# Performance work log

Hardware: AMD Instinct MI355X
Metric: run time of the kernel (lower is better)

Reference implementation:

```python
import jax, jax.numpy as jnp
import numpy as np

P = 4096      # particles per event
F = 128       # max features per particle (inner ragged axis)
H = 128       # hidden_size


def setup_inputs() -> dict:
    key = jax.random.key(0)
    ks = jax.random.split(key, 12)
    s = 1.0 / np.sqrt(H)  # torch RNN default init scale
    u = lambda k, shp: jax.random.uniform(k, shp, jnp.float32, -s, s)
    event = jax.random.normal(ks[0], (P, F, 1), jnp.float32)
    lengths = jnp.maximum(1, jax.random.randint(ks[1], (P,), 0, F))  # ragged lengths in [1, F)
    return {
        "event": event,
        "lengths": lengths,
        "W_ih1": u(ks[2], (H, 1)), "W_hh1": u(ks[3], (H, H)),
        "b_ih1": u(ks[4], (H,)),   "b_hh1": u(ks[5], (H,)),
        "W_ih2": u(ks[6], (H, H)), "W_hh2": u(ks[7], (H, H)),
        "b_ih2": u(ks[8], (H,)),   "b_hh2": u(ks[9], (H,)),
    }


def reference(event, lengths, W_ih1, W_hh1, b_ih1, b_hh1,
              W_ih2, W_hh2, b_ih2, b_hh2):
    # net1: vanilla tanh RNN over each particle's feature sequence (batched over P).
    # Ragged lengths handled by masking the hidden-state update past each length.
    Pn, Fn, _ = event.shape
    mask = jnp.arange(Fn)[:, None] < lengths[None, :]      # [F, P]
    xs = jnp.transpose(event, (1, 0, 2))                   # [F, P, 1] time-major

    def step1(h, xm):
        x, m = xm                                          # x:[P,1], m:[P]
        h_new = jnp.tanh(x @ W_ih1.T + b_ih1 + h @ W_hh1.T + b_hh1)
        return jnp.where(m[:, None], h_new, h), None

    h0 = jnp.zeros((Pn, H), event.dtype)
    h1, _ = jax.lax.scan(step1, h0, (xs, mask))            # final hidden per particle: [P, H]

    # net2: tanh RNN over the sequence of particle hidden states (unbatched).
    def step2(h, x):
        return jnp.tanh(x @ W_ih2.T + b_ih2 + h @ W_hh2.T + b_hh2), None

    h2, _ = jax.lax.scan(step2, jnp.zeros((H,), event.dtype), h1)
    return h2[None, :]                                     # torch hidden shape (1, H)
```

## Files before the change

### kernel.cpp

```cpp
#include <hip/hip_runtime.h>


constexpr int PN = 4096;
constexpr int FN = 128;
constexpr int HN = 128;
constexpr int CH  = 64;
constexpr int NCH = PN / CH;

__device__ __forceinline__ float fast_tanh(float x) {
    float e = __expf(2.0f * x);
    return 1.0f - 2.0f / (e + 1.0f);
}

__device__ __forceinline__ void lds_barrier() {
    asm volatile("s_waitcnt lgkmcnt(0)\n\ts_barrier" ::: "memory");
}

__device__ __forceinline__ float dpp_xor1(float x) {
    return __int_as_float(__builtin_amdgcn_update_dpp(
        0, __float_as_int(x), 0xB1 , 0xF, 0xF, true));
}
__device__ __forceinline__ float dpp_xor2(float x) {
    return __int_as_float(__builtin_amdgcn_update_dpp(
        0, __float_as_int(x), 0x4E , 0xF, 0xF, true));
}
__device__ __forceinline__ float dpp_xor4(float x, bool hi4) {
    int a = __builtin_amdgcn_update_dpp(0, __float_as_int(x), 0x104, 0xF, 0xF, true);
    int b = __builtin_amdgcn_update_dpp(0, __float_as_int(x), 0x114, 0xF, 0xF, true);
    return __int_as_float(hi4 ? b : a);
}

__global__ __launch_bounds__(128) void net1_kernel(
    const float* __restrict__ event,
    const int*   __restrict__ lengths,
    const float* __restrict__ W_ih1,
    const float* __restrict__ W_hh1,
    const float* __restrict__ b_ih1,
    const float* __restrict__ b_hh1,
    const float* __restrict__ W_ih2,
    const float* __restrict__ b_ih2,
    const float* __restrict__ b_hh2,
    float* __restrict__ U)
{
    const int p = blockIdx.x;
    const int i = threadIdx.x;

    __shared__ float h[2][HN];
    __shared__ float ev[FN];

    ev[i]   = event[p * FN + i];
    h[0][i] = 0.0f;

    float w[HN];
    {
        const float4* wrow = reinterpret_cast<const float4*>(W_hh1 + i * HN);
        #pragma unroll
        for (int k = 0; k < HN / 4; ++k) {
            float4 v = wrow[k];
            w[4*k+0] = v.x; w[4*k+1] = v.y; w[4*k+2] = v.z; w[4*k+3] = v.w;
        }
    }
    const float wx   = W_ih1[i];
    const float bias = b_ih1[i] + b_hh1[i];
    const int   len  = lengths[p];

    __syncthreads();

    for (int t = 0; t < len; ++t) {
        const int cur = t & 1;
        const float x = ev[t];
        float a0 = fmaf(wx, x, bias), a1 = 0.f, a2 = 0.f, a3 = 0.f;
        const float4* h4 = reinterpret_cast<const float4*>(h[cur]);
        #pragma unroll
        for (int k = 0; k < HN / 4; ++k) {
            float4 hv = h4[k];
            a0 = fmaf(w[4*k+0], hv.x, a0);
            a1 = fmaf(w[4*k+1], hv.y, a1);
            a2 = fmaf(w[4*k+2], hv.z, a2);
            a3 = fmaf(w[4*k+3], hv.w, a3);
        }
        h[cur ^ 1][i] = fast_tanh((a0 + a1) + (a2 + a3));
        lds_barrier();
    }

    {
        const float4* h4 = reinterpret_cast<const float4*>(h[len & 1]);
        const float4* w2 = reinterpret_cast<const float4*>(W_ih2 + i * HN);
        float a0 = b_ih2[i] + b_hh2[i], a1 = 0.f, a2 = 0.f, a3 = 0.f;
        #pragma unroll
        for (int k = 0; k < HN / 4; ++k) {
            float4 hv = h4[k];
            float4 wv = w2[k];
            a0 = fmaf(wv.x, hv.x, a0);
            a1 = fmaf(wv.y, hv.y, a1);
            a2 = fmaf(wv.z, hv.z, a2);
            a3 = fmaf(wv.w, hv.w, a3);
        }
        U[p * HN + i] = (a0 + a1) + (a2 + a3);
    }
}

__global__ __launch_bounds__(256) void net2_kernel(
    const float* __restrict__ U,
    const float* __restrict__ W_hh2,
    float* __restrict__ out)
{
    const int tid  = threadIdx.x;
    const int wv   = tid >> 6;
    const int lane = tid & 63;
    const int jg   = lane & 7;
    const int ogl  = lane >> 3;
    const int og   = (wv << 3) + ogl;
    const int rot  = jg >> 1;
    const bool hi4 = (jg & 4) != 0;

    const int cidx = ((jg >> 2) & 1) * 2 + ((jg >> 1) & 1);
    const int oi_w = og * 4 + cidx;

    __shared__ float h[2][HN];
    __shared__ float Ulds[2][CH * HN];

    float w[4][16];
    #pragma unroll
    for (int c = 0; c < 4; ++c) {
        const float* row = W_hh2 + (og * 4 + c) * HN + jg * 16;
        #pragma unroll
        for (int t = 0; t < 4; ++t) {
            const int krot = (t + rot) & 3;
            float4 v = *reinterpret_cast<const float4*>(row + 4 * krot);
            w[c][4*t+0] = v.x; w[c][4*t+1] = v.y;
            w[c][4*t+2] = v.z; w[c][4*t+3] = v.w;
        }
    }

    {
        const float4* g = reinterpret_cast<const float4*>(U);
        float4*       l = reinterpret_cast<float4*>(&Ulds[0][0]);
        #pragma unroll
        for (int r = 0; r < 8; ++r) l[r * 256 + tid] = g[r * 256 + tid];
    }
    if (tid < HN) h[0][tid] = 0.0f;
    __syncthreads();

    int buf = 0;
    for (int c = 0; c < NCH; ++c) {
        const int nb = buf ^ 1;

        float4 st[8];
        const int cg = (c + 1 < NCH) ? (c + 1) : c;
        {
            const float4* gsrc = reinterpret_cast<const float4*>(U + cg * CH * HN);
            #pragma unroll
            for (int r = 0; r < 8; ++r) st[r] = gsrc[r * 256 + tid];
        }

        for (int s = 0; s < CH; ++s) {
            const int hc = s & 1;
            const float u_cur = Ulds[buf][s * HN + oi_w];

            const float* base = &h[hc][jg * 16];
            float s0 = 0.f, s1 = 0.f, s2 = 0.f, s3 = 0.f;
            #pragma unroll
            for (int t = 0; t < 4; ++t) {
                const int krot = (t + rot) & 3;
                float4 hv = *reinterpret_cast<const float4*>(base + 4 * krot);
                s0 = fmaf(w[0][4*t+0], hv.x, s0); s0 = fmaf(w[0][4*t+1], hv.y, s0);
                s0 = fmaf(w[0][4*t+2], hv.z, s0); s0 = fmaf(w[0][4*t+3], hv.w, s0);
                s1 = fmaf(w[1][4*t+0], hv.x, s1); s1 = fmaf(w[1][4*t+1], hv.y, s1);
                s1 = fmaf(w[1][4*t+2], hv.z, s1); s1 = fmaf(w[1][4*t+3], hv.w, s1);
                s2 = fmaf(w[2][4*t+0], hv.x, s2); s2 = fmaf(w[2][4*t+1], hv.y, s2);
                s2 = fmaf(w[2][4*t+2], hv.z, s2); s2 = fmaf(w[2][4*t+3], hv.w, s2);
                s3 = fmaf(w[3][4*t+0], hv.x, s3); s3 = fmaf(w[3][4*t+1], hv.y, s3);
                s3 = fmaf(w[3][4*t+2], hv.z, s3); s3 = fmaf(w[3][4*t+3], hv.w, s3);
            }

            const bool lo4 = !hi4;
            float t0 = lo4 ? s2 : s0;
            float t1 = lo4 ? s3 : s1;
            float x0 = (lo4 ? s0 : s2) + dpp_xor4(t0, hi4);
            float x1 = (lo4 ? s1 : s3) + dpp_xor4(t1, hi4);
            const bool lo2 = (jg & 2) == 0;
            float t2 = lo2 ? x1 : x0;
            float z  = (lo2 ? x0 : x1) + dpp_xor2(t2);
            z += dpp_xor1(z);

            const float hn = fast_tanh(z + u_cur);
            if ((jg & 1) == 0) h[hc ^ 1][oi_w] = hn;
            lds_barrier();
        }

        {
            float4* ldst = reinterpret_cast<float4*>(&Ulds[nb][0]);
            #pragma unroll
            for (int r = 0; r < 8; ++r) ldst[r * 256 + tid] = st[r];
        }
        __syncthreads();
        buf = nb;
    }

    if (tid < HN) out[tid] = h[0][tid];

    asm volatile("" :: "v"(w[0][0]));
}

extern "C" void kernel_launch(void* const* d_in, const int* in_sizes, int n_in,
                              void* d_out, int out_size, void* d_ws, size_t ws_size,
                              hipStream_t stream)
{
    const float* event   = (const float*)d_in[0];
    const int*   lengths = (const int*)  d_in[1];
    const float* W_ih1   = (const float*)d_in[2];
    const float* W_hh1   = (const float*)d_in[3];
    const float* b_ih1   = (const float*)d_in[4];
    const float* b_hh1   = (const float*)d_in[5];
    const float* W_ih2   = (const float*)d_in[6];
    const float* W_hh2   = (const float*)d_in[7];
    const float* b_ih2   = (const float*)d_in[8];
    const float* b_hh2   = (const float*)d_in[9];
    float* out = (float*)d_out;
    float* U   = (float*)d_ws;

    hipLaunchKernelGGL(net1_kernel, dim3(PN), dim3(HN), 0, stream,
                       event, lengths, W_ih1, W_hh1, b_ih1, b_hh1,
                       W_ih2, b_ih2, b_hh2, U);
    hipLaunchKernelGGL(net2_kernel, dim3(1), dim3(256), 0, stream,
                       U, W_hh2, out);
}
```

Measured before the change: 1.804 ms.

## Split RNN matvec across 16-lane groups with DPP reduction in both kernels

net1 moves from 128 threads, each holding a full weight row, to 256 threads. Each 16-lane group now computes 8 output rows over 8-element k-slices and combines them with a DPP butterfly reduction (xor 8/4/2/1). This cuts per-thread weight registers from 128 to 64 and the serial FMA chain per step, which should raise occupancy and shorten the per-timestep latency. net2 is changed to the same 8x8 tiling with a 16-lane reduction. The cost is more DPP instructions per step, and the xor-8 row_share/row_xmask DPP path depends on hardware support.

```diff
diff --git a/kernel.cpp b/kernel.cpp
--- a/kernel.cpp
+++ b/kernel.cpp
@@ -24,13 +24,40 @@
     return __int_as_float(__builtin_amdgcn_update_dpp(
         0, __float_as_int(x), 0x4E , 0xF, 0xF, true));
 }
-__device__ __forceinline__ float dpp_xor4(float x, bool hi4) {
+__device__ __forceinline__ float dpp_xor4(float x, bool hi) {
     int a = __builtin_amdgcn_update_dpp(0, __float_as_int(x), 0x104, 0xF, 0xF, true);
     int b = __builtin_amdgcn_update_dpp(0, __float_as_int(x), 0x114, 0xF, 0xF, true);
-    return __int_as_float(hi4 ? b : a);
-}
-
-__global__ __launch_bounds__(128) void net1_kernel(
+    return __int_as_float(hi ? b : a);
+}
+__device__ __forceinline__ float dpp_xor8(float x, bool hi) {
+    int a = __builtin_amdgcn_update_dpp(0, __float_as_int(x), 0x108, 0xF, 0xF, true);
+    int b = __builtin_amdgcn_update_dpp(0, __float_as_int(x), 0x118, 0xF, 0xF, true);
+    return __int_as_float(hi ? b : a);
+}
+
+__device__ __forceinline__ float reduce16(const float s[8], int jg) {
+    const bool hi8 = (jg & 8) != 0;
+    float m0 = hi8 ? s[0] : s[4], k0 = hi8 ? s[4] : s[0];
+    float m1 = hi8 ? s[1] : s[5], k1 = hi8 ? s[5] : s[1];
+    float m2 = hi8 ? s[2] : s[6], k2 = hi8 ? s[6] : s[2];
+    float m3 = hi8 ? s[3] : s[7], k3 = hi8 ? s[7] : s[3];
+    float x0 = k0 + dpp_xor8(m0, hi8);
+    float x1 = k1 + dpp_xor8(m1, hi8);
+    float x2 = k2 + dpp_xor8(m2, hi8);
+    float x3 = k3 + dpp_xor8(m3, hi8);
+    const bool hi4 = (jg & 4) != 0;
+    float y0 = (hi4 ? x2 : x0) + dpp_xor4(hi4 ? x0 : x2, hi4);
+    float y1 = (hi4 ? x3 : x1) + dpp_xor4(hi4 ? x1 : x3, hi4);
+    const bool hi2 = (jg & 2) != 0;
+    float z  = (hi2 ? y1 : y0) + dpp_xor2(hi2 ? y0 : y1);
+    z += dpp_xor1(z);
+    return z;
+}
+__device__ __forceinline__ int reduce16_cidx(int jg) {
+    return ((jg >> 3) & 1) * 4 + ((jg >> 2) & 1) * 2 + ((jg >> 1) & 1);
+}
+
+__global__ __launch_bounds__(256) void net1_kernel(
     const float* __restrict__ event,
     const int*   __restrict__ lengths,
     const float* __restrict__ W_ih1,
@@ -42,51 +69,67 @@
     const float* __restrict__ b_hh2,
     float* __restrict__ U)
 {
-    const int p = blockIdx.x;
-    const int i = threadIdx.x;
+    const int p    = blockIdx.x;
+    const int tid  = threadIdx.x;
+    const int wv   = tid >> 6;
+    const int lane = tid & 63;
+    const int jg   = lane & 15;
+    const int og16 = (wv << 2) + (lane >> 4);
+    const int rot  = (jg >> 2) & 1;
+    const int oi_w = og16 * 8 + reduce16_cidx(jg);
 
     __shared__ float h[2][HN];
     __shared__ float ev[FN];
 
-    ev[i]   = event[p * FN + i];
-    h[0][i] = 0.0f;
-
-    float w[HN];
-    {
-        const float4* wrow = reinterpret_cast<const float4*>(W_hh1 + i * HN);
-        #pragma unroll
-        for (int k = 0; k < HN / 4; ++k) {
-            float4 v = wrow[k];
-            w[4*k+0] = v.x; w[4*k+1] = v.y; w[4*k+2] = v.z; w[4*k+3] = v.w;
-        }
-    }
-    const float wx   = W_ih1[i];
-    const float bias = b_ih1[i] + b_hh1[i];
-    const int   len  = lengths[p];
+    if (tid < FN) ev[tid]   = event[p * FN + tid];
+    if (tid < HN) h[0][tid] = 0.0f;
+
+    float w[8][8];
+    #pragma unroll
+    for (int c = 0; c < 8; ++c) {
+        const float* row = W_hh1 + (og16 * 8 + c) * HN + jg * 8;
+        #pragma unroll
+        for (int t = 0; t < 2; ++t) {
+            const int krot = (t + rot) & 1;
+            float4 v = *reinterpret_cast<const float4*>(row + 4 * krot);
+            w[c][4*t+0] = v.x; w[c][4*t+1] = v.y;
+            w[c][4*t+2] = v.z; w[c][4*t+3] = v.w;
+        }
+    }
+    const float wx_own   = W_ih1[oi_w];
+    const float bias_own = b_ih1[oi_w] + b_hh1[oi_w];
+    const int   len      = lengths[p];
 
     __syncthreads();
 
     for (int t = 0; t < len; ++t) {
         const int cur = t & 1;
         const float x = ev[t];
-        float a0 = fmaf(wx, x, bias), a1 = 0.f, a2 = 0.f, a3 = 0.f;
-        const float4* h4 = reinterpret_cast<const float4*>(h[cur]);
-        #pragma unroll
-        for (int k = 0; k < HN / 4; ++k) {
-            float4 hv = h4[k];
-            a0 = fmaf(w[4*k+0], hv.x, a0);
-            a1 = fmaf(w[4*k+1], hv.y, a1);
-            a2 = fmaf(w[4*k+2], hv.z, a2);
-            a3 = fmaf(w[4*k+3], hv.w, a3);
-        }
-        h[cur ^ 1][i] = fast_tanh((a0 + a1) + (a2 + a3));
+
+        const float* base = &h[cur][jg * 8];
+        float s[8] = {0,0,0,0,0,0,0,0};
+        #pragma unroll
+        for (int tt = 0; tt < 2; ++tt) {
+            const int krot = (tt + rot) & 1;
+            float4 hv = *reinterpret_cast<const float4*>(base + 4 * krot);
+            #pragma unroll
+            for (int c = 0; c < 8; ++c) {
+                s[c] = fmaf(w[c][4*tt+0], hv.x, s[c]);
+                s[c] = fmaf(w[c][4*tt+1], hv.y, s[c]);
+                s[c] = fmaf(w[c][4*tt+2], hv.z, s[c]);
+                s[c] = fmaf(w[c][4*tt+3], hv.w, s[c]);
+            }
+        }
+        const float z  = reduce16(s, jg);
+        const float hn = fast_tanh(z + fmaf(wx_own, x, bias_own));
+        if ((jg & 1) == 0) h[cur ^ 1][oi_w] = hn;
         lds_barrier();
     }
 
-    {
+    if (tid < HN) {
         const float4* h4 = reinterpret_cast<const float4*>(h[len & 1]);
-        const float4* w2 = reinterpret_cast<const float4*>(W_ih2 + i * HN);
-        float a0 = b_ih2[i] + b_hh2[i], a1 = 0.f, a2 = 0.f, a3 = 0.f;
+        const float4* w2 = reinterpret_cast<const float4*>(W_ih2 + tid * HN);
+        float a0 = b_ih2[tid] + b_hh2[tid], a1 = 0.f, a2 = 0.f, a3 = 0.f;
         #pragma unroll
         for (int k = 0; k < HN / 4; ++k) {
             float4 hv = h4[k];
@@ -96,7 +139,7 @@
             a2 = fmaf(wv.z, hv.z, a2);
             a3 = fmaf(wv.w, hv.w, a3);
         }
-        U[p * HN + i] = (a0 + a1) + (a2 + a3);
+        U[p * HN + tid] = (a0 + a1) + (a2 + a3);
     }
 }
 
@@ -108,25 +151,21 @@
     const int tid  = threadIdx.x;
     const int wv   = tid >> 6;
     const int lane = tid & 63;
-    const int jg   = lane & 7;
-    const int ogl  = lane >> 3;
-    const int og   = (wv << 3) + ogl;
-    const int rot  = jg >> 1;
-    const bool hi4 = (jg & 4) != 0;
-
-    const int cidx = ((jg >> 2) & 1) * 2 + ((jg >> 1) & 1);
-    const int oi_w = og * 4 + cidx;
+    const int jg   = lane & 15;
+    const int og16 = (wv << 2) + (lane >> 4);
+    const int rot  = (jg >> 2) & 1;
+    const int oi_w = og16 * 8 + reduce16_cidx(jg);
 
     __shared__ float h[2][HN];
     __shared__ float Ulds[2][CH * HN];
 
-    float w[4][16];
+    float w[8][8];
     #pragma unroll
-    for (int c = 0; c < 4; ++c) {
-        const float* row = W_hh2 + (og * 4 + c) * HN + jg * 16;
-        #pragma unroll
-        for (int t = 0; t < 4; ++t) {
-            const int krot = (t + rot) & 3;
+    for (int c = 0; c < 8; ++c) {
+        const float* row = W_hh2 + (og16 * 8 + c) * HN + jg * 8;
+        #pragma unroll
+        for (int t = 0; t < 2; ++t) {
+            const int krot = (t + rot) & 1;
             float4 v = *reinterpret_cast<const float4*>(row + 4 * krot);
             w[c][4*t+0] = v.x; w[c][4*t+1] = v.y;
             w[c][4*t+2] = v.z; w[c][4*t+3] = v.w;
@@ -154,36 +193,25 @@
             for (int r = 0; r < 8; ++r) st[r] = gsrc[r * 256 + tid];
         }
 
-        for (int s = 0; s < CH; ++s) {
-            const int hc = s & 1;
-            const float u_cur = Ulds[buf][s * HN + oi_w];
-
-            const float* base = &h[hc][jg * 16];
-            float s0 = 0.f, s1 = 0.f, s2 = 0.f, s3 = 0.f;
-            #pragma unroll
-            for (int t = 0; t < 4; ++t) {
-                const int krot = (t + rot) & 3;
+        for (int s2 = 0; s2 < CH; ++s2) {
+            const int hc = s2 & 1;
+            const float u_cur = Ulds[buf][s2 * HN + oi_w];
+
+            const float* base = &h[hc][jg * 8];
+            float s[8] = {0,0,0,0,0,0,0,0};
+            #pragma unroll
+            for (int tt = 0; tt < 2; ++tt) {
+                const int krot = (tt + rot) & 1;
                 float4 hv = *reinterpret_cast<const float4*>(base + 4 * krot);
-                s0 = fmaf(w[0][4*t+0], hv.x, s0); s0 = fmaf(w[0][4*t+1], hv.y, s0);
-                s0 = fmaf(w[0][4*t+2], hv.z, s0); s0 = fmaf(w[0][4*t+3], hv.w, s0);
-                s1 = fmaf(w[1][4*t+0], hv.x, s1); s1 = fmaf(w[1][4*t+1], hv.y, s1);
-                s1 = fmaf(w[1][4*t+2], hv.z, s1); s1 = fmaf(w[1][4*t+3], hv.w, s1);
-                s2 = fmaf(w[2][4*t+0], hv.x, s2); s2 = fmaf(w[2][4*t+1], hv.y, s2);
-                s2 = fmaf(w[2][4*t+2], hv.z, s2); s2 = fmaf(w[2][4*t+3], hv.w, s2);
-                s3 = fmaf(w[3][4*t+0], hv.x, s3); s3 = fmaf(w[3][4*t+1], hv.y, s3);
-                s3 = fmaf(w[3][4*t+2], hv.z, s3); s3 = fmaf(w[3][4*t+3], hv.w, s3);
+                #pragma unroll
+                for (int cc = 0; cc < 8; ++cc) {
+                    s[cc] = fmaf(w[cc][4*tt+0], hv.x, s[cc]);
+                    s[cc] = fmaf(w[cc][4*tt+1], hv.y, s[cc]);
+                    s[cc] = fmaf(w[cc][4*tt+2], hv.z, s[cc]);
+                    s[cc] = fmaf(w[cc][4*tt+3], hv.w, s[cc]);
+                }
             }
-
-            const bool lo4 = !hi4;
-            float t0 = lo4 ? s2 : s0;
-            float t1 = lo4 ? s3 : s1;
-            float x0 = (lo4 ? s0 : s2) + dpp_xor4(t0, hi4);
-            float x1 = (lo4 ? s1 : s3) + dpp_xor4(t1, hi4);
-            const bool lo2 = (jg & 2) == 0;
-            float t2 = lo2 ? x1 : x0;
-            float z  = (lo2 ? x0 : x1) + dpp_xor2(t2);
-            z += dpp_xor1(z);
-
+            const float z  = reduce16(s, jg);
             const float hn = fast_tanh(z + u_cur);
             if ((jg & 1) == 0) h[hc ^ 1][oi_w] = hn;
             lds_barrier();
@@ -199,8 +227,6 @@
     }
 
     if (tid < HN) out[tid] = h[0][tid];
-
-    asm volatile("" :: "v"(w[0][0]));
 }
 
 extern "C" void kernel_launch(void* const* d_in, const int* in_sizes, int n_in,
@@ -220,7 +246,7 @@
     float* out = (float*)d_out;
     float* U   = (float*)d_ws;
 
-    hipLaunchKernelGGL(net1_kernel, dim3(PN), dim3(HN), 0, stream,
+    hipLaunchKernelGGL(net1_kernel, dim3(PN), dim3(256), 0, stream,
                        event, lengths, W_ih1, W_hh1, b_ih1, b_hh1,
                        W_ih2, b_ih2, b_hh2, U);
     hipLaunchKernelGGL(net2_kernel, dim3(1), dim3(256), 0, stream,
```

Measured after the change: 1.875 ms. 3.9% more time.
